# Performance work log

Measured on AMD Instinct MI355X. Metric: run time of the kernel, lower is better.

## Reference

```python
import jax, jax.numpy as jnp
import numpy as np

B, S, D = 4, 2048, 1024
DQ = DK = DV = 1024

def setup_inputs() -> dict:
    key = jax.random.key(0)
    ks = jax.random.split(key, 7)
    s = 1.0 / np.sqrt(D)
    return {
        "X": jax.random.normal(ks[0], (B, S, D), dtype=jnp.float32),
        "Wq": jax.random.normal(ks[1], (D, DQ), dtype=jnp.float32) * s,
        "bq": jax.random.normal(ks[2], (DQ,), dtype=jnp.float32) * 0.01,
        "Wk": jax.random.normal(ks[3], (D, DK), dtype=jnp.float32) * s,
        "bk": jax.random.normal(ks[4], (DK,), dtype=jnp.float32) * 0.01,
        "Wv": jax.random.normal(ks[5], (D, DV), dtype=jnp.float32) * s,
        "bv": jax.random.normal(ks[6], (DV,), dtype=jnp.float32) * 0.01,
    }

def reference(X, Wq, bq, Wk, bk, Wv, bv):
    q = jnp.einsum('bsd,de->bse', X, Wq) + bq  # [B,S,DQ]
    k = jnp.einsum('bsd,de->bse', X, Wk) + bk  # [B,S,DK]
    v = jnp.einsum('bsd,de->bse', X, Wv) + bv  # [B,S,DV]
    scores = jnp.einsum('bqe,bke->bqk', q, k) / jnp.sqrt(jnp.float32(DK))
    attn = jax.nn.softmax(scores, axis=-1)
    return jnp.einsum('bqk,bkv->bqv', attn, v)
```

## Files before the change

### kernel.cpp

```cpp
#include <hip/hip_runtime.h>

typedef __bf16 bf16;
typedef __attribute__((ext_vector_type(8))) __bf16 bf16x8;
typedef __attribute__((ext_vector_type(4))) float f32x4;

typedef __attribute__((address_space(1))) const void GvPtr;
typedef __attribute__((address_space(3))) void LdsPtr;

__device__ __forceinline__ void gload_lds16(const void* g, void* l) {
    __builtin_amdgcn_global_load_lds((GvPtr*)g, (LdsPtr*)l, 16, 0, 0);
}

__global__ __launch_bounds__(256) void prep(
    const void* __restrict__ X,
    const void* __restrict__ Wq, const void* __restrict__ Wk,
    const void* __restrict__ Wv,
    const void* __restrict__ bq, const void* __restrict__ bk,
    const void* __restrict__ bv,
    bf16* __restrict__ Xb, bf16* __restrict__ wt, bf16* __restrict__ bb)
{
    __shared__ int sflag;
    __shared__ bf16 t[32][33];
    const int tid = threadIdx.x;

    if (tid < 64) {
        const unsigned short* H = (const unsigned short*)X;
        int insane = 0;
        for (int i = tid; i < 128; i += 64) {
            int e = (H[2 * i] >> 7) & 0xFF;
            insane += (e >= 107 && e <= 131) ? 0 : 1;
        }
        #pragma unroll
        for (int off = 32; off > 0; off >>= 1)
            insane += __shfl_down(insane, off, 64);
        if (tid == 0) sflag = (insane >= 32) ? 1 : 0;
    }
    __syncthreads();
    const bool isf32 = (sflag != 0);

    const long b = blockIdx.x;
    if (b < 4096) {
        long i = b * 256 + tid;
        if (isf32) {
            const float4* s = (const float4*)X;
            float4 a = s[2 * i], c = s[2 * i + 1];
            bf16x8 o;
            o[0] = (bf16)a.x; o[1] = (bf16)a.y; o[2] = (bf16)a.z; o[3] = (bf16)a.w;
            o[4] = (bf16)c.x; o[5] = (bf16)c.y; o[6] = (bf16)c.z; o[7] = (bf16)c.w;
            ((bf16x8*)Xb)[i] = o;
        } else {
            ((uint4*)Xb)[i] = ((const uint4*)X)[i];
        }
    } else if (b < 7168) {
        const int wi = (int)((b - 4096) >> 10);
        const int id = (int)((b - 4096) & 1023);
        const void* src = (wi == 0) ? Wq : (wi == 1) ? Wk : Wv;
        bf16* dst = wt + (long)wi * 1024 * 1024;
        const int c0 = (id & 31) * 32, r0 = (id >> 5) * 32;
        const int tc = tid & 31, tr = tid >> 5;
        #pragma unroll
        for (int i = 0; i < 4; i++) {
            long idx = (long)(r0 + tr + i * 8) * 1024 + c0 + tc;
            t[tr + i * 8][tc] = isf32 ? (bf16)((const float*)src)[idx]
                                      : ((const bf16*)src)[idx];
        }
        __syncthreads();
        #pragma unroll
        for (int i = 0; i < 4; i++)
            dst[(long)(c0 + tr + i * 8) * 1024 + r0 + tc] = t[tc][tr + i * 8];
    } else {
        const int bi = (int)(b - 7168);
        const int wi = bi >> 2;
        const void* src = (wi == 0) ? bq : (wi == 1) ? bk : bv;
        const long i = (bi & 3) * 256 + tid;
        bb[wi * 1024 + i] = isf32 ? (bf16)((const float*)src)[i]
                                  : ((const bf16*)src)[i];
    }
}

__global__ __launch_bounds__(256) void transpose_bf16s(
    const bf16* __restrict__ src, bf16* __restrict__ dst, int R, int C,
    long srcLd, long srcB, long dstB) {
    __shared__ bf16 t[32][33];
    src += (long)blockIdx.z * srcB;
    dst += (long)blockIdx.z * dstB;
    const int c0 = blockIdx.x * 32, r0 = blockIdx.y * 32;
    const int tc = threadIdx.x & 31, tr = threadIdx.x >> 5;
    #pragma unroll
    for (int i = 0; i < 4; i++)
        t[tr + i * 8][tc] = src[(long)(r0 + tr + i * 8) * srcLd + c0 + tc];
    __syncthreads();
    #pragma unroll
    for (int i = 0; i < 4; i++)
        dst[(long)(c0 + tr + i * 8) * R + r0 + tc] = t[tc][tr + i * 8];
}

template <bool HAS_BIAS, bool OUT_F32, int WAVES>
__global__ __launch_bounds__(WAVES * 64, 4) void gemm_bt(
    const bf16* __restrict__ A, const bf16* __restrict__ B,
    void* __restrict__ Cv, const bf16* __restrict__ bias,
    int K, long lda, long ldb, long ldc, float scale,
    long strideA, long strideB, long strideC)
{
    constexpr int BK = 32;
    constexpr int MI = (WAVES == 4) ? 4 : 2;
    __shared__ bf16 As[128 * BK];
    __shared__ bf16 Bs[128 * BK];

    const int tid  = threadIdx.x;
    const int wave = tid >> 6;
    const int lane = tid & 63;
    const int r16  = lane & 15;
    const int quad = lane >> 4;

    const long z = blockIdx.z;
    A += z * strideA;
    B += z * strideB;

    const int tX = gridDim.x;
    const int pid = blockIdx.y * tX + blockIdx.x;
    const int groupSize = 8 * tX;
    const int gid = pid / groupSize;
    const int rem = pid % groupSize;
    const int tileM = (gid * 8 + (rem & 7)) * 128;
    const int tileN = (rem >> 3) * 128;

    const int waveM = (WAVES == 4) ? (wave >> 1) * 64 : (wave >> 1) * 32;
    const int waveN = (WAVES == 4) ? (wave & 1) * 64 : (wave & 1) * 64;

    const int rowS = tid >> 2;
    const int colS = (tid & 3) * 8;
    const bf16* Ag0 = A + (long)(tileM + rowS) * lda + colS;
    const bf16* Bg0 = B + (long)(tileN + rowS) * ldb + colS;
    const bf16* Ag1 = Ag0 + 64L * lda;
    const bf16* Bg1 = Bg0 + 64L * ldb;
    bf16* AsD0 = &As[tid * 8];
    bf16* BsD0 = &Bs[tid * 8];
    bf16* AsD1 = &As[tid * 8 + 2048];
    bf16* BsD1 = &Bs[tid * 8 + 2048];

    f32x4 acc[MI][4] = {};

    for (int k0 = 0; k0 < K; k0 += BK) {
        gload_lds16(Ag0, AsD0);
        if (WAVES == 4) gload_lds16(Ag1, AsD1);
        gload_lds16(Bg0, BsD0);
        if (WAVES == 4) gload_lds16(Bg1, BsD1);
        Ag0 += BK; Bg0 += BK;
        if (WAVES == 4) { Ag1 += BK; Bg1 += BK; }
        __syncthreads();

        bf16x8 af[MI], bfv[4];
        #pragma unroll
        for (int i = 0; i < MI; i++)
            af[i] = *(const bf16x8*)&As[(waveM + i * 16 + r16) * BK + quad * 8];
        #pragma unroll
        for (int i = 0; i < 4; i++)
            bfv[i] = *(const bf16x8*)&Bs[(waveN + i * 16 + r16) * BK + quad * 8];

        #pragma unroll
        for (int mi = 0; mi < MI; mi++)
            #pragma unroll
            for (int ni = 0; ni < 4; ni++)
                acc[mi][ni] = __builtin_amdgcn_mfma_f32_16x16x32_bf16(
                    af[mi], bfv[ni], acc[mi][ni], 0, 0, 0);
        __syncthreads();
    }

    const int crow0 = tileM + waveM + quad * 4;
    const int ccol0 = tileN + waveN + r16;
    #pragma unroll
    for (int ni = 0; ni < 4; ni++) {
        const int col = ccol0 + ni * 16;
        const float bv = HAS_BIAS ? (float)bias[col] : 0.0f;
        #pragma unroll
        for (int mi = 0; mi < MI; mi++) {
            #pragma unroll
            for (int r = 0; r < 4; r++) {
                const long row = crow0 + mi * 16 + r;
                const float val = acc[mi][ni][r] * scale + bv;
                if (OUT_F32) ((float*)Cv)[z * strideC + row * ldc + col] = val;
                else         ((bf16*)Cv)[z * strideC + row * ldc + col] = (bf16)val;
            }
        }
    }
}

__global__ __launch_bounds__(256) void softmax_rows(
    const bf16* __restrict__ S, bf16* __restrict__ P)
{
    const long row = blockIdx.x;
    const bf16x8* s = (const bf16x8*)(S + row * 2048);
    const int tid = threadIdx.x;

    bf16x8 a = s[tid];
    float v[8];
    float mx = -1e30f;
    #pragma unroll
    for (int i = 0; i < 8; i++) { v[i] = (float)a[i]; mx = fmaxf(mx, v[i]); }
    #pragma unroll
    for (int off = 32; off > 0; off >>= 1)
        mx = fmaxf(mx, __shfl_down(mx, off, 64));
    __shared__ float redm[4];
    if ((tid & 63) == 0) redm[tid >> 6] = mx;
    __syncthreads();
    mx = fmaxf(fmaxf(redm[0], redm[1]), fmaxf(redm[2], redm[3]));

    float sum = 0.0f;
    #pragma unroll
    for (int i = 0; i < 8; i++) { v[i] = __expf(v[i] - mx); sum += v[i]; }
    #pragma unroll
    for (int off = 32; off > 0; off >>= 1)
        sum += __shfl_down(sum, off, 64);
    __shared__ float reds[4];
    if ((tid & 63) == 0) reds[tid >> 6] = sum;
    __syncthreads();
    const float inv = 1.0f / (reds[0] + reds[1] + reds[2] + reds[3]);

    bf16x8 o;
    #pragma unroll
    for (int i = 0; i < 8; i++) o[i] = (bf16)(v[i] * inv);
    ((bf16x8*)(P + row * 2048))[tid] = o;
}

extern "C" void kernel_launch(void* const* d_in, const int* in_sizes, int n_in,
                              void* d_out, int out_size, void* d_ws, size_t ws_size,
                              hipStream_t stream) {
    constexpr int B = 4, S = 2048, D = 1024, N = 1024;
    constexpr long MS = (long)B * S;

    const void* X  = d_in[0];
    const void* Wq = d_in[1];
    const void* bq = d_in[2];
    const void* Wk = d_in[3];
    const void* bk = d_in[4];
    const void* Wv = d_in[5];
    const void* bv = d_in[6];

    char* w = (char*)d_ws;
    bf16* Xb  = (bf16*)w;                w += MS * D * sizeof(bf16);
    bf16* wt  = (bf16*)w;                w += 3L * D * N * sizeof(bf16);
    bf16* bb  = (bf16*)w;                w += 3L * N * sizeof(bf16) + 512;
    bf16* qkv = (bf16*)w;                w += MS * 3L * N * sizeof(bf16);
    bf16* vt  = (bf16*)w;                w += MS * N * sizeof(bf16);
    bf16* sc  = (bf16*)w;                w += (long)B * S * S * sizeof(bf16);
    bf16* pr  = (bf16*)w;

    bf16* q = qkv;
    bf16* k = qkv + N;
    bf16* v = qkv + 2L * N;

    prep<<<7180, 256, 0, stream>>>(X, Wq, Wk, Wv, bq, bk, bv, Xb, wt, bb);

    gemm_bt<true, false, 4><<<dim3(3 * N / 128, MS / 128, 1), 256, 0, stream>>>(
        Xb, wt, qkv, bb, D, D, D, 3L * N, 1.0f, 0, 0, 0);

    gemm_bt<false, false, 4><<<dim3(S / 128, S / 128, B), 256, 0, stream>>>(
        q, k, sc, nullptr, D, 3L * N, 3L * N, S, 0.03125f,
        (long)S * 3 * N, (long)S * 3 * N, (long)S * S);

    softmax_rows<<<B * S, 256, 0, stream>>>(sc, pr);

    transpose_bf16s<<<dim3(N / 32, S / 32, B), 256, 0, stream>>>(
        v, vt, S, N, 3L * N, (long)S * 3 * N, (long)S * N);

    gemm_bt<false, true, 8><<<dim3(N / 128, S / 128, B), 512, 0, stream>>>(
        pr, vt, d_out, nullptr, S, S, S, N, 1.0f,
        (long)S * S, (long)N * S, (long)S * N);
}
```

Baseline: 286.3 us.

## Fuse V transpose into QKV GEMM epilogue and widen K tile with swizzled LDS

The QKV projection GEMM now writes the V columns directly in transposed layout, so the separate transpose kernel and its extra pass over V are removed. The GEMM K tile doubles from 32 to 64 and LDS rows use an XOR-style rotation of the 16-byte chunks to avoid bank conflicts, which halves the number of barriers per K. The larger LDS footprint (32 KB per block) may lower occupancy, and the transposed V stores write 4-element strips with a large stride.

Result: faster. 254.8 us (-11.0%).

```diff
diff --git a/kernel.cpp b/kernel.cpp
--- a/kernel.cpp
+++ b/kernel.cpp
@@ -2,6 +2,7 @@
 
 typedef __bf16 bf16;
 typedef __attribute__((ext_vector_type(8))) __bf16 bf16x8;
+typedef __attribute__((ext_vector_type(4))) __bf16 bf16x4;
 typedef __attribute__((ext_vector_type(4))) float f32x4;
 
 typedef __attribute__((address_space(1))) const void GvPtr;
@@ -78,32 +79,20 @@
     }
 }
 
-__global__ __launch_bounds__(256) void transpose_bf16s(
-    const bf16* __restrict__ src, bf16* __restrict__ dst, int R, int C,
-    long srcLd, long srcB, long dstB) {
-    __shared__ bf16 t[32][33];
-    src += (long)blockIdx.z * srcB;
-    dst += (long)blockIdx.z * dstB;
-    const int c0 = blockIdx.x * 32, r0 = blockIdx.y * 32;
-    const int tc = threadIdx.x & 31, tr = threadIdx.x >> 5;
-    #pragma unroll
-    for (int i = 0; i < 4; i++)
-        t[tr + i * 8][tc] = src[(long)(r0 + tr + i * 8) * srcLd + c0 + tc];
-    __syncthreads();
-    #pragma unroll
-    for (int i = 0; i < 4; i++)
-        dst[(long)(c0 + tr + i * 8) * R + r0 + tc] = t[tc][tr + i * 8];
-}
-
-template <bool HAS_BIAS, bool OUT_F32, int WAVES>
+template <bool HAS_BIAS, bool OUT_F32, int WAVES, bool VSPLIT>
 __global__ __launch_bounds__(WAVES * 64, 4) void gemm_bt(
     const bf16* __restrict__ A, const bf16* __restrict__ B,
     void* __restrict__ Cv, const bf16* __restrict__ bias,
+    bf16* __restrict__ vt,
     int K, long lda, long ldb, long ldc, float scale,
     long strideA, long strideB, long strideC)
 {
-    constexpr int BK = 32;
+    constexpr int BK = 64;
     constexpr int MI = (WAVES == 4) ? 4 : 2;
+    constexpr int NCH = (WAVES == 4) ? 4 : 2;
+    constexpr int RSTEP = WAVES * 8;
+    constexpr int LSTEP = WAVES * 64 * 8;
+
     __shared__ bf16 As[128 * BK];
     __shared__ bf16 Bs[128 * BK];
 
@@ -125,62 +114,89 @@
     const int tileM = (gid * 8 + (rem & 7)) * 128;
     const int tileN = (rem >> 3) * 128;
 
-    const int waveM = (WAVES == 4) ? (wave >> 1) * 64 : (wave >> 1) * 32;
-    const int waveN = (WAVES == 4) ? (wave & 1) * 64 : (wave & 1) * 64;
-
-    const int rowS = tid >> 2;
-    const int colS = (tid & 3) * 8;
-    const bf16* Ag0 = A + (long)(tileM + rowS) * lda + colS;
-    const bf16* Bg0 = B + (long)(tileN + rowS) * ldb + colS;
-    const bf16* Ag1 = Ag0 + 64L * lda;
-    const bf16* Bg1 = Bg0 + 64L * ldb;
-    bf16* AsD0 = &As[tid * 8];
-    bf16* BsD0 = &Bs[tid * 8];
-    bf16* AsD1 = &As[tid * 8 + 2048];
-    bf16* BsD1 = &Bs[tid * 8 + 2048];
+    const int waveM = (wave >> 1) * ((WAVES == 4) ? 64 : 32);
+    const int waveN = (wave & 1) * 64;
+
+    const int rS = tid >> 3;
+    const int cOff = (((tid & 7) - (tid >> 3)) & 7) * 8;
+    const bf16* Ag[NCH]; const bf16* Bg[NCH];
+    #pragma unroll
+    for (int j = 0; j < NCH; j++) {
+        Ag[j] = A + (long)(tileM + rS + j * RSTEP) * lda + cOff;
+        Bg[j] = B + (long)(tileN + rS + j * RSTEP) * ldb + cOff;
+    }
 
     f32x4 acc[MI][4] = {};
 
     for (int k0 = 0; k0 < K; k0 += BK) {
-        gload_lds16(Ag0, AsD0);
-        if (WAVES == 4) gload_lds16(Ag1, AsD1);
-        gload_lds16(Bg0, BsD0);
-        if (WAVES == 4) gload_lds16(Bg1, BsD1);
-        Ag0 += BK; Bg0 += BK;
-        if (WAVES == 4) { Ag1 += BK; Bg1 += BK; }
+        #pragma unroll
+        for (int j = 0; j < NCH; j++) {
+            gload_lds16(Ag[j], &As[tid * 8 + j * LSTEP]);
+            gload_lds16(Bg[j], &Bs[tid * 8 + j * LSTEP]);
+            Ag[j] += BK; Bg[j] += BK;
+        }
         __syncthreads();
 
-        bf16x8 af[MI], bfv[4];
-        #pragma unroll
-        for (int i = 0; i < MI; i++)
-            af[i] = *(const bf16x8*)&As[(waveM + i * 16 + r16) * BK + quad * 8];
-        #pragma unroll
-        for (int i = 0; i < 4; i++)
-            bfv[i] = *(const bf16x8*)&Bs[(waveN + i * 16 + r16) * BK + quad * 8];
-
-        #pragma unroll
-        for (int mi = 0; mi < MI; mi++)
-            #pragma unroll
-            for (int ni = 0; ni < 4; ni++)
-                acc[mi][ni] = __builtin_amdgcn_mfma_f32_16x16x32_bf16(
-                    af[mi], bfv[ni], acc[mi][ni], 0, 0, 0);
+        #pragma unroll
+        for (int ks = 0; ks < 2; ks++) {
+            bf16x8 af[MI], bfv[4];
+            #pragma unroll
+            for (int i = 0; i < MI; i++) {
+                const int row = waveM + i * 16 + r16;
+                af[i] = *(const bf16x8*)
+                    &As[row * 64 + ((ks * 4 + quad + row) & 7) * 8];
+            }
+            #pragma unroll
+            for (int i = 0; i < 4; i++) {
+                const int row = waveN + i * 16 + r16;
+                bfv[i] = *(const bf16x8*)
+                    &Bs[row * 64 + ((ks * 4 + quad + row) & 7) * 8];
+            }
+            #pragma unroll
+            for (int mi = 0; mi < MI; mi++)
+                #pragma unroll
+                for (int ni = 0; ni < 4; ni++)
+                    acc[mi][ni] = __builtin_amdgcn_mfma_f32_16x16x32_bf16(
+                        af[mi], bfv[ni], acc[mi][ni], 0, 0, 0);
+        }
         __syncthreads();
     }
 
     const int crow0 = tileM + waveM + quad * 4;
     const int ccol0 = tileN + waveN + r16;
-    #pragma unroll
-    for (int ni = 0; ni < 4; ni++) {
-        const int col = ccol0 + ni * 16;
-        const float bv = HAS_BIAS ? (float)bias[col] : 0.0f;
-        #pragma unroll
-        for (int mi = 0; mi < MI; mi++) {
-            #pragma unroll
-            for (int r = 0; r < 4; r++) {
-                const long row = crow0 + mi * 16 + r;
-                const float val = acc[mi][ni][r] * scale + bv;
-                if (OUT_F32) ((float*)Cv)[z * strideC + row * ldc + col] = val;
-                else         ((bf16*)Cv)[z * strideC + row * ldc + col] = (bf16)val;
+
+    if (VSPLIT && tileN >= 2048) {
+        #pragma unroll
+        for (int ni = 0; ni < 4; ni++) {
+            const int col = ccol0 + ni * 16;
+            const float bv = HAS_BIAS ? (float)bias[col] : 0.0f;
+            const long colp = col - 2048;
+            #pragma unroll
+            for (int mi = 0; mi < MI; mi++) {
+                const int grow = crow0 + mi * 16;
+                const long bz = grow >> 11;
+                const int srow = grow & 2047;
+                bf16x4 o;
+                #pragma unroll
+                for (int r = 0; r < 4; r++)
+                    o[r] = (bf16)(acc[mi][ni][r] * scale + bv);
+                *(bf16x4*)&vt[(bz << 21) + colp * 2048 + srow] = o;
+            }
+        }
+    } else {
+        #pragma unroll
+        for (int ni = 0; ni < 4; ni++) {
+            const int col = ccol0 + ni * 16;
+            const float bv = HAS_BIAS ? (float)bias[col] : 0.0f;
+            #pragma unroll
+            for (int mi = 0; mi < MI; mi++) {
+                #pragma unroll
+                for (int r = 0; r < 4; r++) {
+                    const long row = crow0 + mi * 16 + r;
+                    const float val = acc[mi][ni][r] * scale + bv;
+                    if (OUT_F32) ((float*)Cv)[z * strideC + row * ldc + col] = val;
+                    else         ((bf16*)Cv)[z * strideC + row * ldc + col] = (bf16)val;
+                }
             }
         }
     }
@@ -248,23 +264,19 @@
 
     bf16* q = qkv;
     bf16* k = qkv + N;
-    bf16* v = qkv + 2L * N;
 
     prep<<<7180, 256, 0, stream>>>(X, Wq, Wk, Wv, bq, bk, bv, Xb, wt, bb);
 
-    gemm_bt<true, false, 4><<<dim3(3 * N / 128, MS / 128, 1), 256, 0, stream>>>(
-        Xb, wt, qkv, bb, D, D, D, 3L * N, 1.0f, 0, 0, 0);
-
-    gemm_bt<false, false, 4><<<dim3(S / 128, S / 128, B), 256, 0, stream>>>(
-        q, k, sc, nullptr, D, 3L * N, 3L * N, S, 0.03125f,
+    gemm_bt<true, false, 4, true><<<dim3(3 * N / 128, MS / 128, 1), 256, 0, stream>>>(
+        Xb, wt, qkv, bb, vt, D, D, D, 3L * N, 1.0f, 0, 0, 0);
+
+    gemm_bt<false, false, 4, false><<<dim3(S / 128, S / 128, B), 256, 0, stream>>>(
+        q, k, sc, nullptr, nullptr, D, 3L * N, 3L * N, S, 0.03125f,
         (long)S * 3 * N, (long)S * 3 * N, (long)S * S);
 
     softmax_rows<<<B * S, 256, 0, stream>>>(sc, pr);
 
-    transpose_bf16s<<<dim3(N / 32, S / 32, B), 256, 0, stream>>>(
-        v, vt, S, N, 3L * N, (long)S * 3 * N, (long)S * N);
-
-    gemm_bt<false, true, 8><<<dim3(N / 128, S / 128, B), 512, 0, stream>>>(
-        pr, vt, d_out, nullptr, S, S, S, N, 1.0f,
+    gemm_bt<false, true, 8, false><<<dim3(N / 128, S / 128, B), 512, 0, stream>>>(
+        pr, vt, d_out, nullptr, nullptr, S, S, S, N, 1.0f,
         (long)S * S, (long)N * S, (long)S * N);
 }
```
